# Kernel optimization log

Hardware: AMD Instinct MI355X
Metric: run time of the kernel (lower is better)

Reference implementation:

```python
import jax, jax.numpy as jnp
import numpy as np

B, T, D, K = 64, 512, 1024, 50


def setup_inputs() -> dict:
    key = jax.random.key(0)
    ks = jax.random.split(key, 6)
    inputs = jax.random.normal(ks[0], (B, T, D), dtype=jnp.float32)
    mask = jnp.ones((B, T), dtype=jnp.int32)
    labels = jax.random.randint(ks[1], (B, T), 0, K)
    W = jax.random.normal(ks[2], (D, K), dtype=jnp.float32) / jnp.sqrt(jnp.float32(D))
    b = jnp.zeros((K,), dtype=jnp.float32)
    transitions = jax.random.normal(ks[3], (K, K), dtype=jnp.float32) * 0.1
    start_transitions = jax.random.normal(ks[4], (K,), dtype=jnp.float32) * 0.1
    end_transitions = jax.random.normal(ks[5], (K,), dtype=jnp.float32) * 0.1
    return dict(inputs=inputs, mask=mask, labels=labels, W=W, b=b,
                transitions=transitions, start_transitions=start_transitions,
                end_transitions=end_transitions)


def _log_partition(emissions, mask_f, trans, start, end):
    # emissions [B,T,K]; forward algorithm with logsumexp recurrence (lax.scan)
    alpha0 = start[None, :] + emissions[:, 0]  # [B,K]
    def step(alpha, xs):
        emit, m = xs  # [B,K], [B]
        inner = alpha[:, :, None] + trans[None, :, :] + emit[:, None, :]  # [B,K,K]
        new = jax.nn.logsumexp(inner, axis=1)
        alpha = jnp.where(m[:, None] > 0, new, alpha)  # carry state through padding
        return alpha, None
    emits = jnp.swapaxes(emissions[:, 1:], 0, 1)  # [T-1,B,K]
    ms = jnp.swapaxes(mask_f[:, 1:], 0, 1)
    alpha, _ = jax.lax.scan(step, alpha0, (emits, ms))
    return jax.nn.logsumexp(alpha + end[None, :], axis=1)  # [B]


def _gold_score(emissions, labels, mask_f, trans, start, end):
    emit_sc = jnp.take_along_axis(emissions, labels[..., None], axis=2)[..., 0]  # [B,T]
    emit_sum = jnp.sum(emit_sc * mask_f, axis=1)
    trans_sc = trans[labels[:, :-1], labels[:, 1:]]  # [B,T-1]
    trans_sum = jnp.sum(trans_sc * mask_f[:, 1:], axis=1)
    last_idx = jnp.sum(mask_f, axis=1).astype(jnp.int32) - 1
    last_tags = jnp.take_along_axis(labels, last_idx[:, None], axis=1)[:, 0]
    return start[labels[:, 0]] + emit_sum + trans_sum + end[last_tags]


def _viterbi(emissions, mask_f, trans, start, end):
    Bv, Tv, Kv = emissions.shape
    alpha0 = start[None, :] + emissions[:, 0]
    ident = jnp.broadcast_to(jnp.arange(Kv, dtype=jnp.int32)[None, :], (Bv, Kv))
    def step(alpha, xs):
        emit, m = xs
        inner = alpha[:, :, None] + trans[None, :, :]  # [B,K_prev,K_cur]
        bp = jnp.argmax(inner, axis=1).astype(jnp.int32)  # [B,K]
        new = jnp.max(inner, axis=1) + emit
        cond = m[:, None] > 0
        alpha = jnp.where(cond, new, alpha)
        bp = jnp.where(cond, bp, ident)  # padded step: tag carries through
        return alpha, bp
    emits = jnp.swapaxes(emissions[:, 1:], 0, 1)
    ms = jnp.swapaxes(mask_f[:, 1:], 0, 1)
    alpha, bps = jax.lax.scan(step, alpha0, (emits, ms))  # bps [T-1,B,K]
    last = jnp.argmax(alpha + end[None, :], axis=1).astype(jnp.int32)  # [B]
    def back(tag, bp):
        prev = jnp.take_along_axis(bp, tag[:, None], axis=1)[:, 0]
        return prev, tag
    first_tag, tags_rest = jax.lax.scan(back, last, bps, reverse=True)  # tags_rest[t]=tag at pos t+1
    tags = jnp.concatenate([first_tag[None, :], tags_rest], axis=0)  # [T,B]
    return jnp.swapaxes(tags, 0, 1)  # [B,T]


def reference(inputs, mask, labels, W, b, transitions, start_transitions, end_transitions):
    emissions = inputs @ W + b  # tag_projection: [B,T,K]
    mask_f = mask.astype(emissions.dtype)
    scores = emissions * mask_f[..., None]  # module masks logits before CRF
    tags = _viterbi(scores, mask_f, transitions, start_transitions, end_transitions)
    tags = tags * mask.astype(tags.dtype)
    ll = _gold_score(scores, labels, mask_f, transitions, start_transitions, end_transitions) \
         - _log_partition(scores, mask_f, transitions, start_transitions, end_transitions)
    loss = -jnp.sum(ll)  # reduction='sum' negative log-likelihood
    return scores, tags, loss
```

## Files before the change

kernel.cpp:

```cpp
#include <hip/hip_runtime.h>

#define B_ 64
#define T_ 512
#define D_ 1024
#define K_ 50
#define MROWS (B_ * T_)

__global__ __launch_bounds__(256) void gemm_kernel(const float* __restrict__ A,
                                                   const float* __restrict__ W,
                                                   float* __restrict__ P0,
                                                   float* __restrict__ P1) {
  __shared__ float As[128][20];
  __shared__ float Wt[52][20];

  const int tid = threadIdx.x;
  const int rowBase = blockIdx.x * 128;
  const int kBase = blockIdx.y * 512;
  float* __restrict__ P = blockIdx.y ? P1 : P0;

  const int rg = tid & 31;
  const int cg = tid >> 5;
  const int c0 = cg * 7;
  const int swr = (rg >> 3) & 3;

  const int q = tid & 3;
  const int rr = tid >> 2;
  const int pA0 = ((q + ((rr >> 3) & 3)) & 3) * 4;
  const int pA1 = ((q + (((rr + 64) >> 3) & 3)) & 3) * 4;
  const int kk0 = tid / 52,         cw0 = tid - kk0 * 52;
  const int kk1 = (tid + 256) / 52, cw1 = tid + 256 - kk1 * 52;
  const int kk2 = (tid + 512) / 52, cw2 = tid + 512 - kk2 * 52;
  const int kk3 = (tid + 768) / 52, cw3 = tid + 768 - kk3 * 52;

  float acc[4][7];
#pragma unroll
  for (int i = 0; i < 4; i++)
#pragma unroll
    for (int j = 0; j < 7; j++) acc[i][j] = 0.f;

  const float* __restrict__ pA0g = &A[(size_t)(rowBase + rr) * 1024 + kBase + q * 4];
  const float* __restrict__ pA1g = &A[(size_t)(rowBase + rr + 64) * 1024 + kBase + q * 4];
  const float* __restrict__ pWg = &W[(size_t)kBase * 50];

  float4 nA0 = *(const float4*)pA0g;
  float4 nA1 = *(const float4*)pA1g;
  float nW0 = (cw0 < 50) ? pWg[(size_t)kk0 * 50 + cw0] : 0.f;
  float nW1 = (cw1 < 50) ? pWg[(size_t)kk1 * 50 + cw1] : 0.f;
  float nW2 = (cw2 < 50) ? pWg[(size_t)kk2 * 50 + cw2] : 0.f;
  float nW3 = (tid < 64 && cw3 < 50) ? pWg[(size_t)kk3 * 50 + cw3] : 0.f;

  for (int ch = 0; ch < 32; ++ch) {
    *(float4*)&As[rr][pA0] = nA0;
    *(float4*)&As[rr + 64][pA1] = nA1;
    Wt[cw0][kk0] = nW0;
    Wt[cw1][kk1] = nW1;
    Wt[cw2][kk2] = nW2;
    if (tid < 64) Wt[cw3][kk3] = nW3;
    __syncthreads();
    if (ch < 31) {
      const int off = (ch + 1) * 16;
      nA0 = *(const float4*)(pA0g + off);
      nA1 = *(const float4*)(pA1g + off);
      const float* pw = pWg + (size_t)off * 50;
      nW0 = (cw0 < 50) ? pw[(size_t)kk0 * 50 + cw0] : 0.f;
      nW1 = (cw1 < 50) ? pw[(size_t)kk1 * 50 + cw1] : 0.f;
      nW2 = (cw2 < 50) ? pw[(size_t)kk2 * 50 + cw2] : 0.f;
      nW3 = (tid < 64 && cw3 < 50) ? pw[(size_t)kk3 * 50 + cw3] : 0.f;
    }
#pragma unroll
    for (int k4 = 0; k4 < 4; k4++) {
      const int pq = ((k4 + swr) & 3) * 4;
      const float4 a0 = *(const float4*)&As[rg][pq];
      const float4 a1 = *(const float4*)&As[rg + 32][pq];
      const float4 a2 = *(const float4*)&As[rg + 64][pq];
      const float4 a3 = *(const float4*)&As[rg + 96][pq];
#pragma unroll
      for (int j = 0; j < 7; j++) {
        const float4 w = *(const float4*)&Wt[c0 + j][k4 * 4];
        float t0 = acc[0][j], t1 = acc[1][j], t2 = acc[2][j], t3 = acc[3][j];
        t0 = fmaf(a0.x, w.x, t0); t1 = fmaf(a1.x, w.x, t1);
        t2 = fmaf(a2.x, w.x, t2); t3 = fmaf(a3.x, w.x, t3);
        t0 = fmaf(a0.y, w.y, t0); t1 = fmaf(a1.y, w.y, t1);
        t2 = fmaf(a2.y, w.y, t2); t3 = fmaf(a3.y, w.y, t3);
        t0 = fmaf(a0.z, w.z, t0); t1 = fmaf(a1.z, w.z, t1);
        t2 = fmaf(a2.z, w.z, t2); t3 = fmaf(a3.z, w.z, t3);
        t0 = fmaf(a0.w, w.w, t0); t1 = fmaf(a1.w, w.w, t1);
        t2 = fmaf(a2.w, w.w, t2); t3 = fmaf(a3.w, w.w, t3);
        acc[0][j] = t0; acc[1][j] = t1; acc[2][j] = t2; acc[3][j] = t3;
      }
    }
    __syncthreads();
  }
#pragma unroll
  for (int j = 0; j < 7; j++) {
    const int c = c0 + j;
    if (c < 50) {
#pragma unroll
      for (int i = 0; i < 4; i++)
        P[(size_t)(rowBase + rg + 32 * i) * 50 + c] = acc[i][j];
    }
  }
}

__global__ __launch_bounds__(256) void combine_kernel(const float* __restrict__ P1,
                                                      const float* __restrict__ bias,
                                                      const int* __restrict__ mask,
                                                      float* __restrict__ scores,
                                                      float* __restrict__ lossSlot) {
  const int idx = blockIdx.x * 256 + threadIdx.x;
  const int m = idx / 50;
  const int c = idx - m * 50;
  const float v = (scores[idx] + P1[idx] + bias[c]) * (float)mask[m];
  scores[idx] = v;
  if (idx == 0) *lossSlot = 0.f;
}

#define PIN4(V) asm volatile("" : "+v"(V.x), "+v"(V.y), "+v"(V.z), "+v"(V.w))

__global__ __launch_bounds__(64, 1) void crf_kernel(const float* __restrict__ scores,
                                                    const int* __restrict__ mask,
                                                    const int* __restrict__ labels,
                                                    const float* __restrict__ trans,
                                                    const float* __restrict__ startT,
                                                    const float* __restrict__ endT,
                                                    float* __restrict__ tagsOut,
                                                    float* __restrict__ lossSlot) {
  __shared__ float x_lds[64];
  __shared__ unsigned char bp_s[511 * 52];
  __shared__ unsigned char g_s[32 * 52];
  __shared__ unsigned char chin_s[32];

  const int b = blockIdx.x;
  const int lane = threadIdx.x;
  const int k = lane;
  const int kc = (k < 50) ? k : 49;
  const size_t sb = (size_t)b * T_ * 50;
  const int bT = b * T_;

  if (blockIdx.y == 0) {
    float4 eTv[13];
#pragma unroll
    for (int u = 0; u < 13; u++) {
      const int j = 4 * u;
      eTv[u].x = (j + 0 < 50) ? __expf(trans[(j + 0) * 50 + kc]) : 0.f;
      eTv[u].y = (j + 1 < 50) ? __expf(trans[(j + 1) * 50 + kc]) : 0.f;
      eTv[u].z = (j + 2 < 50) ? __expf(trans[(j + 2) * 50 + kc]) : 0.f;
      eTv[u].w = (j + 3 < 50) ? __expf(trans[(j + 3) * 50 + kc]) : 0.f;
      PIN4(eTv[u]);
    }
    float af = (k < 50) ? (startT[k] + scores[sb + k]) : -1e30f;
    float M = __int_as_float(__builtin_amdgcn_readfirstlane(__float_as_int(af)));
    float em0 = scores[sb + 50 + kc];
    float em1 = scores[sb + 100 + kc];
    int mk0 = mask[bT + 1];
    int mk1 = mask[bT + 2];
    for (int t = 1; t < T_; ++t) {
      const float emit = em0;
      const int mt = mk0;
      em0 = em1; mk0 = mk1;
      if (t + 2 < T_) {
        em1 = scores[sb + (size_t)(t + 2) * 50 + kc];
        mk1 = mask[bT + t + 2];
      }
      const float e = __expf(af - M);
      x_lds[lane] = e;
      float p0 = 0.f, p1 = 0.f, p2 = 0.f, p3 = 0.f;
#pragma unroll
      for (int u = 0; u < 13; u++) {
        const float4 w = *(const float4*)&x_lds[4 * u];
        p0 = fmaf(w.x, eTv[u].x, p0);
        p1 = fmaf(w.y, eTv[u].y, p1);
        p2 = fmaf(w.z, eTv[u].z, p2);
        p3 = fmaf(w.w, eTv[u].w, p3);
      }
      const float S = (p0 + p1) + (p2 + p3);
      const float afn = M + __logf(S) + emit;
      af = (mt > 0 && k < 50) ? afn : af;
      M = __int_as_float(__builtin_amdgcn_readfirstlane(__float_as_int(af)));
    }
    const float x = (k < 50) ? (af + endT[k]) : -3e38f;
    float mx = x;
#pragma unroll
    for (int off = 32; off >= 1; off >>= 1) mx = fmaxf(mx, __shfl_xor(mx, off));
    float sm = (k < 50) ? __expf(x - mx) : 0.f;
#pragma unroll
    for (int off = 32; off >= 1; off >>= 1) sm += __shfl_xor(sm, off);
    if (lane == 0) atomicAdd(lossSlot, mx + __logf(sm));
  } else if (blockIdx.y == 1) {
    float4 Tv[13];
#pragma unroll
    for (int u = 0; u < 13; u++) {
      const int j = 4 * u;
      Tv[u].x = (j + 0 < 50) ? trans[(j + 0) * 50 + kc] : -1e30f;
      Tv[u].y = (j + 1 < 50) ? trans[(j + 1) * 50 + kc] : -1e30f;
      Tv[u].z = (j + 2 < 50) ? trans[(j + 2) * 50 + kc] : -1e30f;
      Tv[u].w = (j + 3 < 50) ? trans[(j + 3) * 50 + kc] : -1e30f;
      PIN4(Tv[u]);
    }
    float av = (k < 50) ? (startT[k] + scores[sb + k]) : -1e30f;
    float em0 = scores[sb + 50 + kc];
    float em1 = scores[sb + 100 + kc];
    int mk0 = mask[bT + 1];
    int mk1 = mask[bT + 2];
    for (int t = 1; t < T_; ++t) {
      const float emit = em0;
      const int mt = mk0;
      em0 = em1; mk0 = mk1;
      if (t + 2 < T_) {
        em1 = scores[sb + (size_t)(t + 2) * 50 + kc];
        mk1 = mask[bT + t + 2];
      }
      x_lds[lane] = av;
      float4 u0, u1, u2, u3, u4, u5, u6, u7, u8, u9, u10, u11, u12;
      float m13[13];
#define VIT_QUAD(Q, UQ)                                            \
      {                                                            \
        const float4 w = *(const float4*)&x_lds[4 * (Q)];          \
        UQ.x = w.x + Tv[Q].x; UQ.y = w.y + Tv[Q].y;                \
        UQ.z = w.z + Tv[Q].z; UQ.w = w.w + Tv[Q].w;                \
        m13[Q] = fmaxf(fmaxf(UQ.x, UQ.y), fmaxf(UQ.z, UQ.w));      \
      }
      VIT_QUAD(0, u0)   VIT_QUAD(1, u1)   VIT_QUAD(2, u2)
      VIT_QUAD(3, u3)   VIT_QUAD(4, u4)   VIT_QUAD(5, u5)
      VIT_QUAD(6, u6)   VIT_QUAD(7, u7)   VIT_QUAD(8, u8)
      VIT_QUAD(9, u9)   VIT_QUAD(10, u10) VIT_QUAD(11, u11)
      VIT_QUAD(12, u12)
#undef VIT_QUAD
      const float h0 = fmaxf(m13[0], m13[1]);
      const float h1 = fmaxf(m13[2], m13[3]);
      const float h2 = fmaxf(m13[4], m13[5]);
      const float h3 = fmaxf(m13[6], m13[7]);
      const float h4 = fmaxf(m13[8], m13[9]);
      const float h5 = fmaxf(m13[10], m13[11]);
      const float best = fmaxf(fmaxf(fmaxf(h0, h1), fmaxf(h2, h3)),
                               fmaxf(fmaxf(h4, h5), m13[12]));
      int bj = 0;
#define VIT_SCAN(Q, UQ)                                   \
      bj = (UQ.w == best) ? 4 * (Q) + 3 : bj;             \
      bj = (UQ.z == best) ? 4 * (Q) + 2 : bj;             \
      bj = (UQ.y == best) ? 4 * (Q) + 1 : bj;             \
      bj = (UQ.x == best) ? 4 * (Q) + 0 : bj;
      VIT_SCAN(12, u12) VIT_SCAN(11, u11) VIT_SCAN(10, u10)
      VIT_SCAN(9, u9)   VIT_SCAN(8, u8)   VIT_SCAN(7, u7)
      VIT_SCAN(6, u6)   VIT_SCAN(5, u5)   VIT_SCAN(4, u4)
      VIT_SCAN(3, u3)   VIT_SCAN(2, u2)   VIT_SCAN(1, u1)
      VIT_SCAN(0, u0)
#undef VIT_SCAN
      if (k < 50) bp_s[(t - 1) * 52 + k] = (unsigned char)((mt > 0) ? bj : k);
      av = (mt > 0 && k < 50) ? (best + emit) : av;
    }
    float x = (k < 50) ? (av + endT[k]) : -3e38f;
    int xi = (k < 50) ? k : 63;
#pragma unroll
    for (int off = 32; off >= 1; off >>= 1) {
      const float ov = __shfl_xor(x, off);
      const int oi = __shfl_xor(xi, off);
      if (ov > x || (ov == x && oi < xi)) { x = ov; xi = oi; }
    }
    const int last = xi;
    __syncthreads();
#pragma unroll 1
    for (int p = 0; p < 25; p++) {
      const int idx = lane + 64 * p;
      const int c = idx / 50;
      const int s2 = idx - c * 50;
      int x2 = s2;
      const int lo = 16 * c;
      const int hi = min(16 * c + 15, 510);
      for (int i = hi; i >= lo; --i) x2 = bp_s[i * 52 + x2];
      g_s[c * 52 + s2] = (unsigned char)x2;
    }
    __syncthreads();
    if (lane == 0) {
      int cur = last;
      chin_s[31] = (unsigned char)cur;
      for (int c = 31; c >= 1; --c) {
        cur = g_s[c * 52 + cur];
        chin_s[c - 1] = (unsigned char)cur;
      }
      const int m511 = mask[bT + 511];
      tagsOut[(size_t)bT + 511] = (float)((m511 > 0) ? last : 0);
    }
    __syncthreads();
    if (lane < 32) {
      const int c = lane;
      int x3 = chin_s[c];
      const int lo = 16 * c;
      const int hi = min(16 * c + 15, 510);
      for (int i = hi; i >= lo; --i) {
        x3 = bp_s[i * 52 + x3];
        const int mi = mask[bT + i];
        tagsOut[(size_t)bT + i] = (float)((mi > 0) ? x3 : 0);
      }
    }
  } else {
    float part = 0.f;
    int mcnt = 0;
#pragma unroll
    for (int s = 0; s < 8; s++) {
      const int t = lane + 64 * s;
      const int lt = labels[bT + t];
      const int mt = mask[bT + t];
      mcnt += mt;
      if (mt > 0) part += scores[sb + (size_t)t * 50 + lt];
      if (t < T_ - 1) {
        const int ln = labels[bT + t + 1];
        const int mn = mask[bT + t + 1];
        if (mn > 0) part += trans[lt * 50 + ln];
      }
    }
#pragma unroll
    for (int off = 32; off >= 1; off >>= 1) {
      part += __shfl_xor(part, off);
      mcnt += __shfl_xor(mcnt, off);
    }
    if (lane == 0) {
      const int l0 = labels[bT];
      const int llast = labels[bT + (mcnt - 1)];
      const float gold = part + startT[l0] + endT[llast];
      atomicAdd(lossSlot, -gold);
    }
  }
}

extern "C" void kernel_launch(void* const* d_in, const int* in_sizes, int n_in,
                              void* d_out, int out_size, void* d_ws, size_t ws_size,
                              hipStream_t stream) {
  const float* inputs = (const float*)d_in[0];
  const int* mask = (const int*)d_in[1];
  const int* labels = (const int*)d_in[2];
  const float* W = (const float*)d_in[3];
  const float* bias = (const float*)d_in[4];
  const float* trans = (const float*)d_in[5];
  const float* startT = (const float*)d_in[6];
  const float* endT = (const float*)d_in[7];

  float* out = (float*)d_out;
  float* scores = out;
  float* tagsOut = out + (size_t)B_ * T_ * K_;
  float* lossSlot = out + (size_t)B_ * T_ * K_ + B_ * T_;
  float* P1 = (float*)d_ws;

  dim3 g1(MROWS / 128, 2);
  gemm_kernel<<<g1, 256, 0, stream>>>(inputs, W, scores, P1);

  combine_kernel<<<(K_ * MROWS) / 256, 256, 0, stream>>>(P1, bias, mask, scores,
                                                         lossSlot);

  dim3 g3(B_, 3);
  crf_kernel<<<g3, 64, 0, stream>>>(scores, mask, labels, trans, startT, endT,
                                    tagsOut, lossSlot);
}
```

Baseline: 610.4 us.

## Widen GEMM split-K, use readlane broadcasts and ballot masks in CRF recurrences

The GEMM can now split the reduction dimension four ways when the workspace is large enough, and the combine kernel sums all partial buffers. The forward and Viterbi recurrences broadcast alpha across the wavefront with readlane instead of an LDS store and reload, and read the mask from precomputed ballot bitmasks instead of per-step global loads. The Viterbi argmax uses a bitmask plus count-trailing-zeros, and the chunked backtrace walks four chains at once to expose memory-level parallelism. The cost is extra partial-sum traffic in the combine step and many scalar readlane instructions per step.

```diff
diff --git a/kernel.cpp b/kernel.cpp
--- a/kernel.cpp
+++ b/kernel.cpp
@@ -9,14 +9,16 @@
 __global__ __launch_bounds__(256) void gemm_kernel(const float* __restrict__ A,
                                                    const float* __restrict__ W,
                                                    float* __restrict__ P0,
-                                                   float* __restrict__ P1) {
+                                                   float* __restrict__ Pws,
+                                                   int chunkK) {
   __shared__ float As[128][20];
   __shared__ float Wt[52][20];
 
   const int tid = threadIdx.x;
   const int rowBase = blockIdx.x * 128;
-  const int kBase = blockIdx.y * 512;
-  float* __restrict__ P = blockIdx.y ? P1 : P0;
+  const int kBase = blockIdx.y * chunkK;
+  float* __restrict__ P =
+      (blockIdx.y == 0) ? P0 : (Pws + (size_t)(blockIdx.y - 1) * K_ * MROWS);
 
   const int rg = tid & 31;
   const int cg = tid >> 5;
@@ -49,7 +51,8 @@
   float nW2 = (cw2 < 50) ? pWg[(size_t)kk2 * 50 + cw2] : 0.f;
   float nW3 = (tid < 64 && cw3 < 50) ? pWg[(size_t)kk3 * 50 + cw3] : 0.f;
 
-  for (int ch = 0; ch < 32; ++ch) {
+  const int iters = chunkK >> 4;
+  for (int ch = 0; ch < iters; ++ch) {
     *(float4*)&As[rr][pA0] = nA0;
     *(float4*)&As[rr + 64][pA1] = nA1;
     Wt[cw0][kk0] = nW0;
@@ -57,7 +60,7 @@
     Wt[cw2][kk2] = nW2;
     if (tid < 64) Wt[cw3][kk3] = nW3;
     __syncthreads();
-    if (ch < 31) {
+    if (ch < iters - 1) {
       const int off = (ch + 1) * 16;
       nA0 = *(const float4*)(pA0g + off);
       nA1 = *(const float4*)(pA1g + off);
@@ -102,7 +105,8 @@
   }
 }
 
-__global__ __launch_bounds__(256) void combine_kernel(const float* __restrict__ P1,
+__global__ __launch_bounds__(256) void combine_kernel(const float* __restrict__ Pws,
+                                                      int nPart,
                                                       const float* __restrict__ bias,
                                                       const int* __restrict__ mask,
                                                       float* __restrict__ scores,
@@ -110,12 +114,15 @@
   const int idx = blockIdx.x * 256 + threadIdx.x;
   const int m = idx / 50;
   const int c = idx - m * 50;
-  const float v = (scores[idx] + P1[idx] + bias[c]) * (float)mask[m];
-  scores[idx] = v;
+  float s = scores[idx];
+  for (int p = 0; p < nPart; ++p) s += Pws[(size_t)p * K_ * MROWS + idx];
+  s = (s + bias[c]) * (float)mask[m];
+  scores[idx] = s;
   if (idx == 0) *lossSlot = 0.f;
 }
 
 #define PIN4(V) asm volatile("" : "+v"(V.x), "+v"(V.y), "+v"(V.z), "+v"(V.w))
+#define RL(v, J) __int_as_float(__builtin_amdgcn_readlane(__float_as_int(v), (J)))
 
 __global__ __launch_bounds__(64, 1) void crf_kernel(const float* __restrict__ scores,
                                                     const int* __restrict__ mask,
@@ -125,7 +132,6 @@
                                                     const float* __restrict__ endT,
                                                     float* __restrict__ tagsOut,
                                                     float* __restrict__ lossSlot) {
-  __shared__ float x_lds[64];
   __shared__ unsigned char bp_s[511 * 52];
   __shared__ unsigned char g_s[32 * 52];
   __shared__ unsigned char chin_s[32];
@@ -136,6 +142,15 @@
   const int kc = (k < 50) ? k : 49;
   const size_t sb = (size_t)b * T_ * 50;
   const int bT = b * T_;
+
+  const unsigned long long bm0 = __ballot(mask[bT + 0 * 64 + lane] > 0);
+  const unsigned long long bm1 = __ballot(mask[bT + 1 * 64 + lane] > 0);
+  const unsigned long long bm2 = __ballot(mask[bT + 2 * 64 + lane] > 0);
+  const unsigned long long bm3 = __ballot(mask[bT + 3 * 64 + lane] > 0);
+  const unsigned long long bm4 = __ballot(mask[bT + 4 * 64 + lane] > 0);
+  const unsigned long long bm5 = __ballot(mask[bT + 5 * 64 + lane] > 0);
+  const unsigned long long bm6 = __ballot(mask[bT + 6 * 64 + lane] > 0);
+  const unsigned long long bm7 = __ballot(mask[bT + 7 * 64 + lane] > 0);
 
   if (blockIdx.y == 0) {
     float4 eTv[13];
@@ -152,32 +167,46 @@
     float M = __int_as_float(__builtin_amdgcn_readfirstlane(__float_as_int(af)));
     float em0 = scores[sb + 50 + kc];
     float em1 = scores[sb + 100 + kc];
-    int mk0 = mask[bT + 1];
-    int mk1 = mask[bT + 2];
-    for (int t = 1; t < T_; ++t) {
-      const float emit = em0;
-      const int mt = mk0;
-      em0 = em1; mk0 = mk1;
-      if (t + 2 < T_) {
-        em1 = scores[sb + (size_t)(t + 2) * 50 + kc];
-        mk1 = mask[bT + t + 2];
-      }
-      const float e = __expf(af - M);
-      x_lds[lane] = e;
-      float p0 = 0.f, p1 = 0.f, p2 = 0.f, p3 = 0.f;
-#pragma unroll
-      for (int u = 0; u < 13; u++) {
-        const float4 w = *(const float4*)&x_lds[4 * u];
-        p0 = fmaf(w.x, eTv[u].x, p0);
-        p1 = fmaf(w.y, eTv[u].y, p1);
-        p2 = fmaf(w.z, eTv[u].z, p2);
-        p3 = fmaf(w.w, eTv[u].w, p3);
-      }
-      const float S = (p0 + p1) + (p2 + p3);
-      const float afn = M + __logf(S) + emit;
-      af = (mt > 0 && k < 50) ? afn : af;
-      M = __int_as_float(__builtin_amdgcn_readfirstlane(__float_as_int(af)));
-    }
+
+#define FWD_Q(U)                                        \
+    p0 = fmaf(RL(e, 4 * (U) + 0), eTv[U].x, p0);        \
+    p1 = fmaf(RL(e, 4 * (U) + 1), eTv[U].y, p1);        \
+    p2 = fmaf(RL(e, 4 * (U) + 2), eTv[U].z, p2);        \
+    p3 = fmaf(RL(e, 4 * (U) + 3), eTv[U].w, p3);
+
+#define FWD_BODY(T, BMV)                                             \
+    {                                                                \
+      const int t = (T);                                             \
+      const float emit = em0;                                        \
+      em0 = em1;                                                     \
+      if (t + 2 < T_) em1 = scores[sb + (size_t)(t + 2) * 50 + kc];  \
+      const int mt = (int)(((BMV) >> (t & 63)) & 1ull);              \
+      const float e = __expf(af - M);                                \
+      float p0 = 0.f, p1 = 0.f, p2 = 0.f, p3 = 0.f;                  \
+      FWD_Q(0) FWD_Q(1) FWD_Q(2) FWD_Q(3) FWD_Q(4) FWD_Q(5)          \
+      FWD_Q(6) FWD_Q(7) FWD_Q(8) FWD_Q(9) FWD_Q(10) FWD_Q(11)        \
+      FWD_Q(12)                                                      \
+      const float S = (p0 + p1) + (p2 + p3);                         \
+      const float afn = M + __logf(S) + emit;                        \
+      af = (mt && k < 50) ? afn : af;                                \
+      M = __int_as_float(__builtin_amdgcn_readfirstlane(__float_as_int(af))); \
+    }
+
+#define FWD_PHASE(P, BMV, T0)                       \
+    _Pragma("unroll 1")                             \
+    for (int tt = (T0); tt < 64; ++tt) {            \
+      FWD_BODY((P) * 64 + tt, BMV)                  \
+    }
+
+    FWD_PHASE(0, bm0, 1)
+    FWD_PHASE(1, bm1, 0)
+    FWD_PHASE(2, bm2, 0)
+    FWD_PHASE(3, bm3, 0)
+    FWD_PHASE(4, bm4, 0)
+    FWD_PHASE(5, bm5, 0)
+    FWD_PHASE(6, bm6, 0)
+    FWD_PHASE(7, bm7, 0)
+
     const float x = (k < 50) ? (af + endT[k]) : -3e38f;
     float mx = x;
 #pragma unroll
@@ -200,55 +229,73 @@
     float av = (k < 50) ? (startT[k] + scores[sb + k]) : -1e30f;
     float em0 = scores[sb + 50 + kc];
     float em1 = scores[sb + 100 + kc];
-    int mk0 = mask[bT + 1];
-    int mk1 = mask[bT + 2];
-    for (int t = 1; t < T_; ++t) {
-      const float emit = em0;
-      const int mt = mk0;
-      em0 = em1; mk0 = mk1;
-      if (t + 2 < T_) {
-        em1 = scores[sb + (size_t)(t + 2) * 50 + kc];
-        mk1 = mask[bT + t + 2];
-      }
-      x_lds[lane] = av;
-      float4 u0, u1, u2, u3, u4, u5, u6, u7, u8, u9, u10, u11, u12;
-      float m13[13];
-#define VIT_QUAD(Q, UQ)                                            \
-      {                                                            \
-        const float4 w = *(const float4*)&x_lds[4 * (Q)];          \
-        UQ.x = w.x + Tv[Q].x; UQ.y = w.y + Tv[Q].y;                \
-        UQ.z = w.z + Tv[Q].z; UQ.w = w.w + Tv[Q].w;                \
-        m13[Q] = fmaxf(fmaxf(UQ.x, UQ.y), fmaxf(UQ.z, UQ.w));      \
-      }
-      VIT_QUAD(0, u0)   VIT_QUAD(1, u1)   VIT_QUAD(2, u2)
-      VIT_QUAD(3, u3)   VIT_QUAD(4, u4)   VIT_QUAD(5, u5)
-      VIT_QUAD(6, u6)   VIT_QUAD(7, u7)   VIT_QUAD(8, u8)
-      VIT_QUAD(9, u9)   VIT_QUAD(10, u10) VIT_QUAD(11, u11)
-      VIT_QUAD(12, u12)
-#undef VIT_QUAD
-      const float h0 = fmaxf(m13[0], m13[1]);
-      const float h1 = fmaxf(m13[2], m13[3]);
-      const float h2 = fmaxf(m13[4], m13[5]);
-      const float h3 = fmaxf(m13[6], m13[7]);
-      const float h4 = fmaxf(m13[8], m13[9]);
-      const float h5 = fmaxf(m13[10], m13[11]);
-      const float best = fmaxf(fmaxf(fmaxf(h0, h1), fmaxf(h2, h3)),
-                               fmaxf(fmaxf(h4, h5), m13[12]));
-      int bj = 0;
-#define VIT_SCAN(Q, UQ)                                   \
-      bj = (UQ.w == best) ? 4 * (Q) + 3 : bj;             \
-      bj = (UQ.z == best) ? 4 * (Q) + 2 : bj;             \
-      bj = (UQ.y == best) ? 4 * (Q) + 1 : bj;             \
-      bj = (UQ.x == best) ? 4 * (Q) + 0 : bj;
-      VIT_SCAN(12, u12) VIT_SCAN(11, u11) VIT_SCAN(10, u10)
-      VIT_SCAN(9, u9)   VIT_SCAN(8, u8)   VIT_SCAN(7, u7)
-      VIT_SCAN(6, u6)   VIT_SCAN(5, u5)   VIT_SCAN(4, u4)
-      VIT_SCAN(3, u3)   VIT_SCAN(2, u2)   VIT_SCAN(1, u1)
-      VIT_SCAN(0, u0)
-#undef VIT_SCAN
-      if (k < 50) bp_s[(t - 1) * 52 + k] = (unsigned char)((mt > 0) ? bj : k);
-      av = (mt > 0 && k < 50) ? (best + emit) : av;
-    }
+
+#define VIT_Q(U, UQ, MQ)                                          \
+    float4 UQ; float MQ;                                          \
+    UQ.x = RL(av, 4 * (U) + 0) + Tv[U].x;                         \
+    UQ.y = RL(av, 4 * (U) + 1) + Tv[U].y;                         \
+    UQ.z = RL(av, 4 * (U) + 2) + Tv[U].z;                         \
+    UQ.w = RL(av, 4 * (U) + 3) + Tv[U].w;                         \
+    MQ = fmaxf(fmaxf(UQ.x, UQ.y), fmaxf(UQ.z, UQ.w));
+
+#define SCAN_LO(U, UQ)                                            \
+    lo |= (UQ.x == best) ? (1u << (4 * (U) + 0)) : 0u;            \
+    lo |= (UQ.y == best) ? (1u << (4 * (U) + 1)) : 0u;            \
+    lo |= (UQ.z == best) ? (1u << (4 * (U) + 2)) : 0u;            \
+    lo |= (UQ.w == best) ? (1u << (4 * (U) + 3)) : 0u;
+
+#define SCAN_HI(U, UQ)                                            \
+    hi |= (UQ.x == best) ? (1u << (4 * (U) - 32)) : 0u;           \
+    hi |= (UQ.y == best) ? (1u << (4 * (U) - 31)) : 0u;           \
+    hi |= (UQ.z == best) ? (1u << (4 * (U) - 30)) : 0u;           \
+    hi |= (UQ.w == best) ? (1u << (4 * (U) - 29)) : 0u;
+
+#define VIT_BODY(T, BMV)                                             \
+    {                                                                \
+      const int t = (T);                                             \
+      const float emit = em0;                                        \
+      em0 = em1;                                                     \
+      if (t + 2 < T_) em1 = scores[sb + (size_t)(t + 2) * 50 + kc];  \
+      const int mt = (int)(((BMV) >> (t & 63)) & 1ull);              \
+      VIT_Q(0, u0, q0)  VIT_Q(1, u1, q1)   VIT_Q(2, u2, q2)          \
+      VIT_Q(3, u3, q3)  VIT_Q(4, u4, q4)   VIT_Q(5, u5, q5)          \
+      VIT_Q(6, u6, q6)  VIT_Q(7, u7, q7)   VIT_Q(8, u8, q8)          \
+      VIT_Q(9, u9, q9)  VIT_Q(10, u10, q10) VIT_Q(11, u11, q11)      \
+      VIT_Q(12, u12, q12)                                            \
+      const float h0 = fmaxf(q0, q1);                                \
+      const float h1 = fmaxf(q2, q3);                                \
+      const float h2 = fmaxf(q4, q5);                                \
+      const float h3 = fmaxf(q6, q7);                                \
+      const float h4 = fmaxf(q8, q9);                                \
+      const float h5 = fmaxf(q10, q11);                              \
+      const float best = fmaxf(fmaxf(fmaxf(h0, h1), fmaxf(h2, h3)),  \
+                               fmaxf(fmaxf(h4, h5), q12));           \
+      unsigned lo = 0u, hi = 0u;                                     \
+      SCAN_LO(0, u0) SCAN_LO(1, u1) SCAN_LO(2, u2) SCAN_LO(3, u3)    \
+      SCAN_LO(4, u4) SCAN_LO(5, u5) SCAN_LO(6, u6) SCAN_LO(7, u7)    \
+      SCAN_HI(8, u8) SCAN_HI(9, u9) SCAN_HI(10, u10) SCAN_HI(11, u11)\
+      SCAN_HI(12, u12)                                               \
+      const int bj = (lo != 0u) ? __builtin_ctz(lo)                  \
+                                : 32 + __builtin_ctz(hi);            \
+      if (k < 50) bp_s[(t - 1) * 52 + k] = (unsigned char)(mt ? bj : k); \
+      av = (mt && k < 50) ? (best + emit) : av;                      \
+    }
+
+#define VIT_PHASE(P, BMV, T0)                       \
+    _Pragma("unroll 1")                             \
+    for (int tt = (T0); tt < 64; ++tt) {            \
+      VIT_BODY((P) * 64 + tt, BMV)                  \
+    }
+
+    VIT_PHASE(0, bm0, 1)
+    VIT_PHASE(1, bm1, 0)
+    VIT_PHASE(2, bm2, 0)
+    VIT_PHASE(3, bm3, 0)
+    VIT_PHASE(4, bm4, 0)
+    VIT_PHASE(5, bm5, 0)
+    VIT_PHASE(6, bm6, 0)
+    VIT_PHASE(7, bm7, 0)
+
     float x = (k < 50) ? (av + endT[k]) : -3e38f;
     int xi = (k < 50) ? k : 63;
 #pragma unroll
@@ -260,15 +307,38 @@
     const int last = xi;
     __syncthreads();
 #pragma unroll 1
-    for (int p = 0; p < 25; p++) {
-      const int idx = lane + 64 * p;
-      const int c = idx / 50;
-      const int s2 = idx - c * 50;
-      int x2 = s2;
-      const int lo = 16 * c;
-      const int hi = min(16 * c + 15, 510);
-      for (int i = hi; i >= lo; --i) x2 = bp_s[i * 52 + x2];
-      g_s[c * 52 + s2] = (unsigned char)x2;
+    for (int g = 0; g < 6; ++g) {
+      const int iA = lane + 64 * (4 * g + 0);
+      const int iB = lane + 64 * (4 * g + 1);
+      const int iC = lane + 64 * (4 * g + 2);
+      const int iD = lane + 64 * (4 * g + 3);
+      const int cA = iA / 50, sA = iA - 50 * cA;
+      const int cB = iB / 50, sB = iB - 50 * cB;
+      const int cC = iC / 50, sC = iC - 50 * cC;
+      const int cD = iD / 50, sD = iD - 50 * cD;
+      int xA = sA, xB = sB, xC = sC, xD = sD;
+#pragma unroll 1
+      for (int i = 15; i >= 0; --i) {
+        xA = bp_s[(16 * cA + i) * 52 + xA];
+        xB = bp_s[(16 * cB + i) * 52 + xB];
+        xC = bp_s[(16 * cC + i) * 52 + xC];
+        xD = bp_s[(16 * cD + i) * 52 + xD];
+      }
+      g_s[cA * 52 + sA] = (unsigned char)xA;
+      g_s[cB * 52 + sB] = (unsigned char)xB;
+      g_s[cC * 52 + sC] = (unsigned char)xC;
+      g_s[cD * 52 + sD] = (unsigned char)xD;
+    }
+    {
+      const int iE = lane + 1536;
+      const int cE = iE / 50, sE = iE - 50 * cE;
+      int xE = sE;
+#pragma unroll 1
+      for (int i = 15; i >= 0; --i) {
+        const int r = 16 * cE + i;
+        if (r <= 510) xE = bp_s[r * 52 + xE];
+      }
+      g_s[cE * 52 + sE] = (unsigned char)xE;
     }
     __syncthreads();
     if (lane == 0) {
@@ -285,9 +355,9 @@
     if (lane < 32) {
       const int c = lane;
       int x3 = chin_s[c];
-      const int lo = 16 * c;
-      const int hi = min(16 * c + 15, 510);
-      for (int i = hi; i >= lo; --i) {
+      const int lo2 = 16 * c;
+      const int hi2 = min(16 * c + 15, 510);
+      for (int i = hi2; i >= lo2; --i) {
         x3 = bp_s[i * 52 + x3];
         const int mi = mask[bT + i];
         tagsOut[(size_t)bT + i] = (float)((mi > 0) ? x3 : 0);
@@ -339,13 +409,17 @@
   float* scores = out;
   float* tagsOut = out + (size_t)B_ * T_ * K_;
   float* lossSlot = out + (size_t)B_ * T_ * K_ + B_ * T_;
-  float* P1 = (float*)d_ws;
-
-  dim3 g1(MROWS / 128, 2);
-  gemm_kernel<<<g1, 256, 0, stream>>>(inputs, W, scores, P1);
-
-  combine_kernel<<<(K_ * MROWS) / 256, 256, 0, stream>>>(P1, bias, mask, scores,
-                                                         lossSlot);
+  float* Pws = (float*)d_ws;
+
+  const size_t per = (size_t)K_ * MROWS * sizeof(float);
+  const int SK = (ws_size >= 3 * per) ? 4 : 2;
+  const int chunkK = D_ / SK;
+
+  dim3 g1(MROWS / 128, SK);
+  gemm_kernel<<<g1, 256, 0, stream>>>(inputs, W, scores, Pws, chunkK);
+
+  combine_kernel<<<(K_ * MROWS) / 256, 256, 0, stream>>>(Pws, SK - 1, bias, mask,
+                                                         scores, lossSlot);
 
   dim3 g3(B_, 3);
   crf_kernel<<<g3, 64, 0, stream>>>(scores, mask, labels, trans, startT, endT,
```

After: 580.8 us. 4.9% less time.
